# Kernel tuning notes

Measured on AMD Instinct MI355X. Metric: run time of the kernel, lower is better.

The kernel has to match this reference:

```python
import jax, jax.numpy as jnp
import numpy as np

EMBED_DIM = 1024
NUM_HEADS = 16
BLOCK_SIZE = 128
GLOBAL_EVERY = 24


def make_block_sparse_mask(seq_len):
    # 0 where allowed, -inf where disallowed. Allowed iff same block, or
    # either position lies in a 'global' block (block index % global_every == 0).
    bi = jnp.arange(seq_len) // BLOCK_SIZE
    is_global = (bi % GLOBAL_EVERY) == 0
    allowed = (bi[:, None] == bi[None, :]) | is_global[:, None] | is_global[None, :]
    return jnp.where(allowed, 0.0, -jnp.inf).astype(jnp.float32)


def setup_inputs() -> dict:
    key = jax.random.key(0)
    k_x, k_w, k_wo = jax.random.split(key, 3)
    B, L, D = 1, 4096, EMBED_DIM
    x = jax.random.normal(k_x, (B, L, D), dtype=jnp.float32)
    # nn.MultiheadAttention params: packed in_proj [3D, D] + bias [3D], out_proj [D, D] + bias [D]
    w_qkv = jax.random.normal(k_w, (3 * D, D), dtype=jnp.float32) * 0.02
    b_qkv = jnp.zeros((3 * D,), dtype=jnp.float32)
    w_out = jax.random.normal(k_wo, (D, D), dtype=jnp.float32) * 0.02
    b_out = jnp.zeros((D,), dtype=jnp.float32)
    return {"x": x, "w_qkv": w_qkv, "b_qkv": b_qkv, "w_out": w_out, "b_out": b_out}


def reference(x, w_qkv, b_qkv, w_out, b_out):
    B, L, D = x.shape
    H = NUM_HEADS
    hd = D // H
    mask = make_block_sparse_mask(L)  # [L, L] additive
    qkv = x @ w_qkv.T + b_qkv  # [B, L, 3D]
    q, k, v = jnp.split(qkv, 3, axis=-1)
    # [B, H, L, hd]
    q = q.reshape(B, L, H, hd).transpose(0, 2, 1, 3)
    k = k.reshape(B, L, H, hd).transpose(0, 2, 1, 3)
    v = v.reshape(B, L, H, hd).transpose(0, 2, 1, 3)
    scale = 1.0 / jnp.sqrt(jnp.asarray(hd, dtype=x.dtype))
    scores = jnp.einsum('bhqd,bhkd->bhqk', q * scale, k) + mask  # [B, H, L, L]
    attn = jax.nn.softmax(scores, axis=-1)
    out = jnp.einsum('bhqk,bhkd->bhqd', attn, v)  # [B, H, L, hd]
    out = out.transpose(0, 2, 1, 3).reshape(B, L, D)
    return out @ w_out.T + b_out
```

## Files before the change

### kernel.cpp

```cpp
#include <hip/hip_runtime.h>
#include <hip/hip_bf16.h>
#include <math.h>


#define SEQ 4096
#define DIM 1024
#define NHEADS 16
#define HDIM 64
#define BS 128
#define ESTRIDE 136

using short8 = __attribute__((ext_vector_type(8))) short;
using floatx4 = __attribute__((ext_vector_type(4))) float;

__device__ __forceinline__ float bf2f(short s) {
  unsigned u = ((unsigned)(unsigned short)s) << 16;
  return __uint_as_float(u);
}

__device__ __forceinline__ unsigned pack_bf16(float a, float b) {
  __hip_bfloat16 ba = __float2bfloat16(a);
  __hip_bfloat16 bb = __float2bfloat16(b);
  return ((unsigned)*(unsigned short*)&bb << 16) | (unsigned)*(unsigned short*)&ba;
}

__device__ __forceinline__ void gld_lds16(const __hip_bfloat16* g, __hip_bfloat16* l) {
  __builtin_amdgcn_global_load_lds(
      (const __attribute__((address_space(1))) unsigned int*)g,
      (__attribute__((address_space(3))) unsigned int*)l, 16, 0, 0);
}

__global__ __launch_bounds__(256) void downcast3(
    const float* __restrict__ x, const float* __restrict__ wq,
    const float* __restrict__ wo, __hip_bfloat16* __restrict__ xd,
    __hip_bfloat16* __restrict__ wqd, __hip_bfloat16* __restrict__ wod) {
  int id = blockIdx.x;
  const float* src;
  __hip_bfloat16* dst;
  int base;
  if (id < 4096) { src = x; dst = xd; base = id; }
  else if (id < 7168) { src = wq; dst = wqd; base = id - 4096; }
  else { src = wo; dst = wod; base = id - 7168; }
  int i = (base * 256 + threadIdx.x) * 4;
  float4 v = *(const float4*)(src + i);
  __hip_bfloat16 b0 = __float2bfloat16(v.x);
  __hip_bfloat16 b1 = __float2bfloat16(v.y);
  __hip_bfloat16 b2 = __float2bfloat16(v.z);
  __hip_bfloat16 b3 = __float2bfloat16(v.w);
  ushort4 packed = {*(unsigned short*)&b0, *(unsigned short*)&b1,
                    *(unsigned short*)&b2, *(unsigned short*)&b3};
  *(ushort4*)(((unsigned short*)dst) + i) = packed;
}

__global__ __launch_bounds__(256) void gemm_qkv(const __hip_bfloat16* __restrict__ Amat,
                                                const __hip_bfloat16* __restrict__ Wmat,
                                                const float* __restrict__ Bias,
                                                __hip_bfloat16* __restrict__ qkv) {
  __shared__ __align__(16) char pool[128 * ESTRIDE * 2];
  __hip_bfloat16* Asmem = (__hip_bfloat16*)pool;
  __hip_bfloat16* Bsmem = (__hip_bfloat16*)(pool + 8192);
  __hip_bfloat16* Ep = (__hip_bfloat16*)pool;

  const int Kd = DIM;
  const int t = threadIdx.x;
  const int w = t >> 6;
  const int lane = t & 63;
  const int fr = lane & 15;
  const int quad = lane >> 4;
  const int wm = w >> 1, wn = w & 1;

  int id = blockIdx.x;
  int xcd = id & 7, j = id >> 3;
  int m_idx = xcd + (j & 3) * 8;
  int n_idx = j >> 2;
  const int m0 = m_idx * 128;
  const int n0 = n_idx * 128;
  const int s = n0 >> 10;
  const int cc0 = n0 & 1023;
  const bool vmode = (s == 2);

  const __hip_bfloat16* APtr = vmode ? Amat + (size_t)m0 * Kd : Wmat + (size_t)n0 * Kd;
  const __hip_bfloat16* BPtr = vmode ? Wmat + (size_t)n0 * Kd : Amat + (size_t)m0 * Kd;

  floatx4 acc[4][4];
#pragma unroll
  for (int i = 0; i < 4; ++i)
#pragma unroll
    for (int jj = 0; jj < 4; ++jj) acc[i][jj] = (floatx4){0.f, 0.f, 0.f, 0.f};

  for (int kk = 0; kk < Kd / 32; ++kk) {
#pragma unroll
    for (int jj = 0; jj < 2; ++jj) {
      int c = jj * 256 + t;
      int ldso = (jj * 256 + w * 64) * 8;
      gld_lds16(APtr + (size_t)(c >> 2) * Kd + kk * 32 + (c & 3) * 8, &Asmem[ldso]);
      gld_lds16(BPtr + (size_t)(c >> 2) * Kd + kk * 32 + (c & 3) * 8, &Bsmem[ldso]);
    }
    __syncthreads();
    short8 af[4], bf_[4];
#pragma unroll
    for (int mt = 0; mt < 4; ++mt)
      af[mt] = *(const short8*)&Asmem[(wm * 64 + mt * 16 + fr) * 32 + quad * 8];
#pragma unroll
    for (int nt = 0; nt < 4; ++nt)
      bf_[nt] = *(const short8*)&Bsmem[(wn * 64 + nt * 16 + fr) * 32 + quad * 8];
#pragma unroll
    for (int mt = 0; mt < 4; ++mt)
#pragma unroll
      for (int nt = 0; nt < 4; ++nt)
        acc[mt][nt] = __builtin_amdgcn_mfma_f32_16x16x32_bf16(af[mt], bf_[nt],
                                                              acc[mt][nt], 0, 0, 0);
    __syncthreads();
  }

#pragma unroll
  for (int nt = 0; nt < 4; ++nt) {
    int dcol = wn * 64 + nt * 16 + fr;
#pragma unroll
    for (int mt = 0; mt < 4; ++mt) {
      int drow0 = wm * 64 + mt * 16 + quad * 4;
      ushort4 pk;
      unsigned short* pks = (unsigned short*)&pk;
#pragma unroll
      for (int i = 0; i < 4; ++i) {
        __hip_bfloat16 bb = __float2bfloat16(acc[mt][nt][i]);
        pks[i] = *(unsigned short*)&bb;
      }
      *(ushort4*)&Ep[dcol * ESTRIDE + drow0] = pk;
    }
  }
  __syncthreads();

  if (!vmode) {
    __hip_bfloat16* dst = qkv + (size_t)s * SEQ * DIM;
#pragma unroll
    for (int rr = 0; rr < 8; ++rr) {
      int m = rr * 16 + (t >> 4);
      int ch = (t & 15) * 8;
      short8 v8 = *(const short8*)&Ep[m * ESTRIDE + ch];
      float4 b0 = *(const float4*)&Bias[n0 + ch];
      float4 b1 = *(const float4*)&Bias[n0 + ch + 4];
      float bb[8] = {b0.x, b0.y, b0.z, b0.w, b1.x, b1.y, b1.z, b1.w};
      short8 o8;
#pragma unroll
      for (int k = 0; k < 8; ++k) {
        __hip_bfloat16 ob = __float2bfloat16(bf2f(v8[k]) + bb[k]);
        o8[k] = *(short*)&ob;
      }
      *(short8*)&dst[(size_t)(m0 + m) * DIM + cc0 + ch] = o8;
    }
  } else {
    __hip_bfloat16* vt = qkv + 2ull * SEQ * DIM;
#pragma unroll
    for (int rr = 0; rr < 8; ++rr) {
      int nrow = rr * 16 + (t >> 4);
      int ch = (t & 15) * 8;
      float bv = Bias[n0 + nrow];
      short8 v8 = *(const short8*)&Ep[nrow * ESTRIDE + ch];
      short8 o8;
#pragma unroll
      for (int k = 0; k < 8; ++k) {
        __hip_bfloat16 ob = __float2bfloat16(bf2f(v8[k]) + bv);
        o8[k] = *(short*)&ob;
      }
      *(short8*)&vt[(size_t)(cc0 + nrow) * SEQ + m0 + ch] = o8;
    }
  }
}

__global__ __launch_bounds__(256) void gemm_out(const __hip_bfloat16* __restrict__ Amat,
                                                const __hip_bfloat16* __restrict__ Wmat,
                                                const float* __restrict__ Bias,
                                                float* __restrict__ out) {
  __shared__ __align__(16) __hip_bfloat16 Asmem[128 * 32];
  __shared__ __align__(16) __hip_bfloat16 Bsmem[64 * 32];
  const int Kd = DIM;
  const int t = threadIdx.x;
  const int w = t >> 6;
  const int lane = t & 63;
  const int fr = lane & 15;
  const int quad = lane >> 4;
  const int wm = w >> 1, wn = w & 1;
  int id = blockIdx.x;
  int xcd = id & 7, j = id >> 3;
  int m_idx = xcd + (j & 3) * 8;
  int n_idx = j >> 2;
  const int m0 = m_idx * 128;
  const int n0 = n_idx * 64;
  const __hip_bfloat16* Ablk = Amat + (size_t)m0 * Kd;
  const __hip_bfloat16* Bblk = Wmat + (size_t)n0 * Kd;
  floatx4 acc[4][2];
#pragma unroll
  for (int i = 0; i < 4; ++i)
#pragma unroll
    for (int jj = 0; jj < 2; ++jj) acc[i][jj] = (floatx4){0.f, 0.f, 0.f, 0.f};
  for (int kk = 0; kk < Kd / 32; ++kk) {
#pragma unroll
    for (int jj = 0; jj < 2; ++jj) {
      int c = jj * 256 + t;
      int ldso = (jj * 256 + w * 64) * 8;
      gld_lds16(Ablk + (size_t)(c >> 2) * Kd + kk * 32 + (c & 3) * 8, &Asmem[ldso]);
    }
    gld_lds16(Bblk + (size_t)(t >> 2) * Kd + kk * 32 + (t & 3) * 8, &Bsmem[t * 8]);
    __syncthreads();
    short8 af[4], bf_[2];
#pragma unroll
    for (int mt = 0; mt < 4; ++mt)
      af[mt] = *(const short8*)&Asmem[(wm * 64 + mt * 16 + fr) * 32 + quad * 8];
#pragma unroll
    for (int nt = 0; nt < 2; ++nt)
      bf_[nt] = *(const short8*)&Bsmem[(wn * 32 + nt * 16 + fr) * 32 + quad * 8];
#pragma unroll
    for (int mt = 0; mt < 4; ++mt)
#pragma unroll
      for (int nt = 0; nt < 2; ++nt)
        acc[mt][nt] = __builtin_amdgcn_mfma_f32_16x16x32_bf16(af[mt], bf_[nt],
                                                              acc[mt][nt], 0, 0, 0);
    __syncthreads();
  }
#pragma unroll
  for (int nt = 0; nt < 2; ++nt) {
    int n = n0 + wn * 32 + nt * 16 + fr;
    float bv = Bias[n];
#pragma unroll
    for (int mt = 0; mt < 4; ++mt) {
      int m = m0 + wm * 64 + mt * 16 + quad * 4;
#pragma unroll
      for (int i = 0; i < 4; ++i)
        out[(size_t)(m + i) * DIM + n] = acc[mt][nt][i] + bv;
    }
  }
}

__global__ __launch_bounds__(256) void attn_mfma(
    const __hip_bfloat16* __restrict__ qkv,
    __hip_bfloat16* __restrict__ aout,
    float* __restrict__ po, float* __restrict__ pm, float* __restrict__ pl) {
  __shared__ __align__(16) __hip_bfloat16 Kbuf[16 * 512];
  __shared__ __align__(16) __hip_bfloat16 Vbuf[16 * 512];
  const int h = blockIdx.y;
  const int wgid = blockIdx.x;
  const int t = threadIdx.x;
  const int wv = t >> 6;
  const int lane = t & 63;
  const int fr = lane & 15;
  const int quad = lane >> 4;

  int qb, q0, niter, slice = 0, pid = 0;
  bool direct;
  if (wgid < 60) {
    int nb = wgid >> 1;
    qb = (nb < 23) ? nb + 1 : nb + 2;
    q0 = qb * BS + (wgid & 1) * 64;
    niter = 3;
    direct = true;
  } else {
    int gi = wgid - 60;
    slice = gi & 7;
    int chunk = gi >> 3;
    qb = (chunk >> 1) * 24;
    q0 = qb * BS + (chunk & 1) * 64;
    niter = 4;
    direct = false;
    pid = (h * 4 + chunk) * 8 + slice;
  }

  const __hip_bfloat16* Q = qkv;
  const __hip_bfloat16* K = qkv + (size_t)SEQ * DIM;
  const __hip_bfloat16* Vt = qkv + 2ull * SEQ * DIM;

  short8 qa0, qa1;
  {
    const __hip_bfloat16* qp =
        Q + (size_t)(q0 + wv * 16 + fr) * DIM + h * HDIM + quad * 8;
    qa0 = *(const short8*)(qp);
    qa1 = *(const short8*)(qp + 32);
  }

  float mrow = -INFINITY, lsum = 0.f;
  floatx4 o[4];
#pragma unroll
  for (int i = 0; i < 4; ++i) o[i] = (floatx4){0.f, 0.f, 0.f, 0.f};

  for (int bi = 0; bi < niter; ++bi) {
    int kb = direct ? (bi == 0 ? 0 : (bi == 1 ? qb : 24)) : slice * 4 + bi;

    const __hip_bfloat16* Kg = K + (size_t)(kb * BS) * DIM + h * HDIM;
    const __hip_bfloat16* Vg = Vt + (size_t)(h * HDIM) * SEQ + kb * BS;
    __syncthreads();
#pragma unroll
    for (int rr = 0; rr < 4; ++rr) {
      int f = rr * 4 + wv;
      int nt = f >> 1, ks = f & 1;
      gld_lds16(Kg + (size_t)(nt * 16 + fr) * DIM + ks * 32 + quad * 8,
                &Kbuf[f * 512]);
      int nt2 = f >> 2, ks2 = f & 3;
      gld_lds16(Vg + (size_t)(nt2 * 16 + fr) * SEQ + ks2 * 32 + quad * 8,
                &Vbuf[f * 512]);
    }
    __syncthreads();

    floatx4 s[8];
#pragma unroll
    for (int nt = 0; nt < 8; ++nt) {
      short8 kf0 = *(const short8*)&Kbuf[(nt * 2 + 0) * 512 + lane * 8];
      short8 kf1 = *(const short8*)&Kbuf[(nt * 2 + 1) * 512 + lane * 8];
      floatx4 acc = {0.f, 0.f, 0.f, 0.f};
      acc = __builtin_amdgcn_mfma_f32_16x16x32_bf16(kf0, qa0, acc, 0, 0, 0);
      acc = __builtin_amdgcn_mfma_f32_16x16x32_bf16(kf1, qa1, acc, 0, 0, 0);
      s[nt] = acc;
    }
#pragma unroll
    for (int nt = 0; nt < 8; ++nt)
#pragma unroll
      for (int i = 0; i < 4; ++i) s[nt][i] *= 0.125f;

    float rmax = -INFINITY;
#pragma unroll
    for (int nt = 0; nt < 8; ++nt)
#pragma unroll
      for (int i = 0; i < 4; ++i) rmax = fmaxf(rmax, s[nt][i]);
    rmax = fmaxf(rmax, __shfl_xor(rmax, 16, 64));
    rmax = fmaxf(rmax, __shfl_xor(rmax, 32, 64));
    float newm = fmaxf(mrow, rmax);
    float alpha = __expf(mrow - newm);
    float psum = 0.f;
    unsigned pki[8][2];
#pragma unroll
    for (int nt = 0; nt < 8; ++nt) {
      float p0 = __expf(s[nt][0] - newm);
      float p1 = __expf(s[nt][1] - newm);
      float p2 = __expf(s[nt][2] - newm);
      float p3 = __expf(s[nt][3] - newm);
      psum += (p0 + p1) + (p2 + p3);
      pki[nt][0] = pack_bf16(p0, p1);
      pki[nt][1] = pack_bf16(p2, p3);
    }
    psum += __shfl_xor(psum, 16, 64);
    psum += __shfl_xor(psum, 32, 64);
    lsum = lsum * alpha + psum;
    mrow = newm;
#pragma unroll
    for (int nt2 = 0; nt2 < 4; ++nt2)
#pragma unroll
      for (int i = 0; i < 4; ++i) o[nt2][i] *= alpha;

    union { int w4[4]; short8 s8; } pw[4];
#pragma unroll
    for (int ks2 = 0; ks2 < 4; ++ks2) {
#pragma unroll
      for (int p = 0; p < 4; ++p) {
        int srcl = fr + ((((quad & 1) << 1) + (p >> 1)) << 4);
        int lo = __shfl((int)pki[2 * ks2][p & 1], srcl, 64);
        int hi = __shfl((int)pki[2 * ks2 + 1][p & 1], srcl, 64);
        pw[ks2].w4[p] = (quad & 2) ? hi : lo;
      }
    }

#pragma unroll
    for (int nt2 = 0; nt2 < 4; ++nt2) {
#pragma unroll
      for (int ks2 = 0; ks2 < 4; ++ks2) {
        short8 vb = *(const short8*)&Vbuf[(nt2 * 4 + ks2) * 512 + lane * 8];
        o[nt2] = __builtin_amdgcn_mfma_f32_16x16x32_bf16(vb, pw[ks2].s8, o[nt2], 0, 0, 0);
      }
    }
  }

  if (direct) {
    float inv = 1.f / lsum;
    __hip_bfloat16* orow = aout + (size_t)(q0 + wv * 16 + fr) * DIM + h * HDIM + quad * 4;
#pragma unroll
    for (int nt2 = 0; nt2 < 4; ++nt2) {
      ushort4 pk;
      unsigned short* pks = (unsigned short*)&pk;
#pragma unroll
      for (int i = 0; i < 4; ++i) {
        __hip_bfloat16 ob = __float2bfloat16(o[nt2][i] * inv);
        pks[i] = *(unsigned short*)&ob;
      }
      *(ushort4*)(orow + nt2 * 16) = pk;
    }
  } else {
    float* pob = po + (size_t)pid * 4096 + (wv * 16 + fr) * 64 + quad * 4;
#pragma unroll
    for (int nt2 = 0; nt2 < 4; ++nt2) {
      float4 v = {o[nt2][0], o[nt2][1], o[nt2][2], o[nt2][3]};
      *(float4*)(pob + nt2 * 16) = v;
    }
    if (quad == 0) {
      pm[pid * 64 + wv * 16 + fr] = mrow;
      pl[pid * 64 + wv * 16 + fr] = lsum;
    }
  }
}

__global__ __launch_bounds__(256) void combine(const float* __restrict__ po,
                                               const float* __restrict__ pm,
                                               const float* __restrict__ pl,
                                               __hip_bfloat16* __restrict__ aout) {
  int b = blockIdx.x;
  int h = b >> 2, chunk = b & 3;
  int t = threadIdx.x;
  int row = t >> 2;
  int d0 = (t & 3) * 16;

  float m8[8];
  float newm = -INFINITY;
#pragma unroll
  for (int s = 0; s < 8; ++s) {
    m8[s] = pm[(b * 8 + s) * 64 + row];
    newm = fmaxf(newm, m8[s]);
  }
  float wgt[8], lsum = 0.f;
#pragma unroll
  for (int s = 0; s < 8; ++s) {
    wgt[s] = __expf(m8[s] - newm);
    lsum += pl[(b * 8 + s) * 64 + row] * wgt[s];
  }
  float acc[16];
#pragma unroll
  for (int jj = 0; jj < 16; ++jj) acc[jj] = 0.f;
#pragma unroll
  for (int s = 0; s < 8; ++s) {
    const float* src = po + ((size_t)(b * 8 + s) * 4096) + row * 64 + d0;
#pragma unroll
    for (int j4 = 0; j4 < 4; ++j4) {
      float4 v = *(const float4*)(src + j4 * 4);
      acc[j4 * 4 + 0] += wgt[s] * v.x;
      acc[j4 * 4 + 1] += wgt[s] * v.y;
      acc[j4 * 4 + 2] += wgt[s] * v.z;
      acc[j4 * 4 + 3] += wgt[s] * v.w;
    }
  }
  float inv = 1.f / lsum;
  int qrow = (chunk >> 1) * 3072 + (chunk & 1) * 64 + row;
#pragma unroll
  for (int jj = 0; jj < 16; ++jj)
    aout[(size_t)qrow * DIM + h * HDIM + d0 + jj] = __float2bfloat16(acc[jj] * inv);
}

extern "C" void kernel_launch(void* const* d_in, const int* in_sizes, int n_in,
                              void* d_out, int out_size, void* d_ws, size_t ws_size,
                              hipStream_t stream) {
  const float* x = (const float*)d_in[0];
  const float* w_qkv = (const float*)d_in[1];
  const float* b_qkv = (const float*)d_in[2];
  const float* w_out = (const float*)d_in[3];
  const float* b_out = (const float*)d_in[4];
  float* out = (float*)d_out;

  char* wsb = (char*)d_ws;
  __hip_bfloat16* qkv_ws = (__hip_bfloat16*)(wsb);
  __hip_bfloat16* x_bf = (__hip_bfloat16*)(wsb + 24ull * 1024 * 1024);
  __hip_bfloat16* wqkv_bf = (__hip_bfloat16*)(wsb + 32ull * 1024 * 1024);
  __hip_bfloat16* wout_bf = (__hip_bfloat16*)(wsb + 38ull * 1024 * 1024);
  __hip_bfloat16* attn_ws = (__hip_bfloat16*)(wsb + 40ull * 1024 * 1024);
  float* po = (float*)(wsb + 24ull * 1024 * 1024);
  float* pm = (float*)(wsb + 32ull * 1024 * 1024);
  float* pl = (float*)(wsb + 32ull * 1024 * 1024 + 131072);

  dim3 blk(256);
  downcast3<<<dim3(8192), blk, 0, stream>>>(x, w_qkv, w_out, x_bf, wqkv_bf, wout_bf);
  gemm_qkv<<<dim3(768), blk, 0, stream>>>(x_bf, wqkv_bf, b_qkv, qkv_ws);
  attn_mfma<<<dim3(92, NHEADS), blk, 0, stream>>>(qkv_ws, attn_ws, po, pm, pl);
  combine<<<dim3(64), blk, 0, stream>>>(po, pm, pl, attn_ws);
  gemm_out<<<dim3(512), blk, 0, stream>>>(attn_ws, wout_bf, b_out, out);
}
```

Before: 175.1 us.

## Load K/V fragments directly from global memory, dropping LDS staging and barriers

The attention kernel no longer stages K and V tiles through shared memory with two barriers per iteration. Each wave now reads its MFMA fragments straight from global memory, and four waves in a workgroup read the same K/V data redundantly, relying on L2/L1 caching. The softmax scale is also folded into the exp argument through an fma, with a tree-shaped max reduction. This removes the separate scale pass and syncs, but adds redundant, less-coalesced global traffic.

```diff
diff --git a/kernel.cpp b/kernel.cpp
--- a/kernel.cpp
+++ b/kernel.cpp
@@ -236,8 +236,6 @@
     const __hip_bfloat16* __restrict__ qkv,
     __hip_bfloat16* __restrict__ aout,
     float* __restrict__ po, float* __restrict__ pm, float* __restrict__ pl) {
-  __shared__ __align__(16) __hip_bfloat16 Kbuf[16 * 512];
-  __shared__ __align__(16) __hip_bfloat16 Vbuf[16 * 512];
   const int h = blockIdx.y;
   const int wgid = blockIdx.x;
   const int t = threadIdx.x;
@@ -284,54 +282,42 @@
 
   for (int bi = 0; bi < niter; ++bi) {
     int kb = direct ? (bi == 0 ? 0 : (bi == 1 ? qb : 24)) : slice * 4 + bi;
-
-    const __hip_bfloat16* Kg = K + (size_t)(kb * BS) * DIM + h * HDIM;
-    const __hip_bfloat16* Vg = Vt + (size_t)(h * HDIM) * SEQ + kb * BS;
-    __syncthreads();
-#pragma unroll
-    for (int rr = 0; rr < 4; ++rr) {
-      int f = rr * 4 + wv;
-      int nt = f >> 1, ks = f & 1;
-      gld_lds16(Kg + (size_t)(nt * 16 + fr) * DIM + ks * 32 + quad * 8,
-                &Kbuf[f * 512]);
-      int nt2 = f >> 2, ks2 = f & 3;
-      gld_lds16(Vg + (size_t)(nt2 * 16 + fr) * SEQ + ks2 * 32 + quad * 8,
-                &Vbuf[f * 512]);
-    }
-    __syncthreads();
+    const __hip_bfloat16* kr =
+        K + (size_t)(kb * BS + fr) * DIM + h * HDIM + quad * 8;
+    const __hip_bfloat16* vr =
+        Vt + (size_t)(h * HDIM + fr) * SEQ + kb * BS + quad * 8;
 
     floatx4 s[8];
 #pragma unroll
     for (int nt = 0; nt < 8; ++nt) {
-      short8 kf0 = *(const short8*)&Kbuf[(nt * 2 + 0) * 512 + lane * 8];
-      short8 kf1 = *(const short8*)&Kbuf[(nt * 2 + 1) * 512 + lane * 8];
+      short8 kf0 = *(const short8*)(kr + (size_t)nt * 16 * DIM);
+      short8 kf1 = *(const short8*)(kr + (size_t)nt * 16 * DIM + 32);
       floatx4 acc = {0.f, 0.f, 0.f, 0.f};
       acc = __builtin_amdgcn_mfma_f32_16x16x32_bf16(kf0, qa0, acc, 0, 0, 0);
       acc = __builtin_amdgcn_mfma_f32_16x16x32_bf16(kf1, qa1, acc, 0, 0, 0);
       s[nt] = acc;
     }
+
+    float mr[8];
 #pragma unroll
     for (int nt = 0; nt < 8; ++nt)
-#pragma unroll
-      for (int i = 0; i < 4; ++i) s[nt][i] *= 0.125f;
-
-    float rmax = -INFINITY;
-#pragma unroll
-    for (int nt = 0; nt < 8; ++nt)
-#pragma unroll
-      for (int i = 0; i < 4; ++i) rmax = fmaxf(rmax, s[nt][i]);
+      mr[nt] = fmaxf(fmaxf(s[nt][0], s[nt][1]), fmaxf(s[nt][2], s[nt][3]));
+    float m01 = fmaxf(mr[0], mr[1]), m23 = fmaxf(mr[2], mr[3]);
+    float m45 = fmaxf(mr[4], mr[5]), m67 = fmaxf(mr[6], mr[7]);
+    float rmax = fmaxf(fmaxf(m01, m23), fmaxf(m45, m67));
     rmax = fmaxf(rmax, __shfl_xor(rmax, 16, 64));
     rmax = fmaxf(rmax, __shfl_xor(rmax, 32, 64));
     float newm = fmaxf(mrow, rmax);
-    float alpha = __expf(mrow - newm);
+    float alpha = __expf((mrow - newm) * 0.125f);
+    float nm = newm * 0.125f;
     float psum = 0.f;
     unsigned pki[8][2];
 #pragma unroll
     for (int nt = 0; nt < 8; ++nt) {
-      float p0 = __expf(s[nt][0] - newm);
-      float p1 = __expf(s[nt][1] - newm);
-      float p2 = __expf(s[nt][2] - newm);
-      float p3 = __expf(s[nt][3] - newm);
+      float p0 = __expf(fmaf(s[nt][0], 0.125f, -nm));
+      float p1 = __expf(fmaf(s[nt][1], 0.125f, -nm));
+      float p2 = __expf(fmaf(s[nt][2], 0.125f, -nm));
+      float p3 = __expf(fmaf(s[nt][3], 0.125f, -nm));
       psum += (p0 + p1) + (p2 + p3);
       pki[nt][0] = pack_bf16(p0, p1);
       pki[nt][1] = pack_bf16(p2, p3);
@@ -361,7 +347,7 @@
     for (int nt2 = 0; nt2 < 4; ++nt2) {
 #pragma unroll
       for (int ks2 = 0; ks2 < 4; ++ks2) {
-        short8 vb = *(const short8*)&Vbuf[(nt2 * 4 + ks2) * 512 + lane * 8];
+        short8 vb = *(const short8*)(vr + (size_t)nt2 * 16 * SEQ + ks2 * 32);
         o[nt2] = __builtin_amdgcn_mfma_f32_16x16x32_bf16(vb, pw[ks2].s8, o[nt2], 0, 0, 0);
       }
     }
@@ -389,7 +375,7 @@
       *(float4*)(pob + nt2 * 16) = v;
     }
     if (quad == 0) {
-      pm[pid * 64 + wv * 16 + fr] = mrow;
+      pm[pid * 64 + wv * 16 + fr] = mrow * 0.125f;
       pl[pid * 64 + wv * 16 + fr] = lsum;
     }
   }
```

Measured after the change: 224.6 us. 1.28x slower.
